# Performance work log

Measured on AMD Instinct MI355X. Metric: run time of the kernel, lower is better.

Reference implementation:

```python
import jax, jax.numpy as jnp
import numpy as np

B, N, EB, NA, DIM, NIT = 256, 128, 5, 64, 512, 3  # EB = n_bonds + 1 (channel 0 = no-bond, dropped)


def setup_inputs() -> dict:
    key = jax.random.key(0)
    ks = jax.random.split(key, 10)
    adj = jax.random.uniform(ks[0], (B, N, N, EB), dtype=jnp.float32)
    node = jax.random.normal(ks[1], (B, N, NA), dtype=jnp.float32)
    hidden = jnp.zeros((B, N, DIM), dtype=jnp.float32)  # accepted but unused by forward
    # nn.Linear default init: U(-1/sqrt(fan_in), 1/sqrt(fan_in))
    se = 1.0 / np.sqrt(NA)
    sd = 1.0 / np.sqrt(DIM)
    W_embed = jax.random.uniform(ks[2], (NA, DIM), minval=-se, maxval=se, dtype=jnp.float32)
    b_embed = jax.random.uniform(ks[3], (DIM,), minval=-se, maxval=se, dtype=jnp.float32)
    W_layers = jax.random.uniform(ks[4], (NIT, DIM, DIM), minval=-sd, maxval=sd, dtype=jnp.float32)
    b_layers = jax.random.uniform(ks[5], (NIT, DIM), minval=-sd, maxval=sd, dtype=jnp.float32)
    W_out = jax.random.uniform(ks[6], (DIM, 1), minval=-sd, maxval=sd, dtype=jnp.float32)
    b_out = jax.random.uniform(ks[7], (1,), minval=-sd, maxval=sd, dtype=jnp.float32)
    return {"adj": adj, "hidden": hidden, "node": node,
            "W_embed": W_embed, "b_embed": b_embed,
            "W_layers": W_layers, "b_layers": b_layers,
            "W_out": W_out, "b_out": b_out}


def reference(adj, hidden, node, W_embed, b_embed, W_layers, b_layers, W_out, b_out):
    # adj[:, :, :, 1:].permute(0, 3, 1, 2) -> [B, E, N, N]
    a = jnp.transpose(adj[..., 1:], (0, 3, 1, 2))
    h = node @ W_embed + b_embed  # [B, N, DIM]
    for i in range(NIT):  # WLSLinearLayer: relu(Linear(h + sum_e adj_e @ h))
        agg = jnp.einsum('benm,bmd->bnd', a, h)  # sum over bond types of neighbor aggregation
        h = jax.nn.relu((h + agg) @ W_layers[i] + b_layers[i])
    graph_repr = jnp.mean(h, axis=1)  # [B, DIM]
    logit = graph_repr @ W_out + b_out  # [B, 1], activation=None path
    return (logit, graph_repr)
```

## Files before the change

kernel.cpp:

```cpp
#include <hip/hip_runtime.h>
#include <hip/hip_bf16.h>


typedef __bf16 bf16;
typedef __bf16 bf16x4 __attribute__((ext_vector_type(4)));
typedef __bf16 bf16x8 __attribute__((ext_vector_type(8)));
typedef float floatx4 __attribute__((ext_vector_type(4)));

#define TBS 40
#define AS  136

__global__ __launch_bounds__(256) void k_pack(const float* __restrict__ We,
                                              const float* __restrict__ Wl,
                                              bf16* __restrict__ PWe,
                                              bf16* __restrict__ PWl) {
    __shared__ float S[512][17];
    int z = blockIdx.y, td = blockIdx.x;
    const float* src; bf16* dst; int K;
    if (z < 3) { src = Wl + (size_t)z * 262144; dst = PWl + (size_t)z * 262144; K = 512; }
    else       { src = We;                      dst = PWe;                      K = 64; }
    int tid = threadIdx.x;
    int x = tid & 15, y = tid >> 4;
    for (int kb = 0; kb < K; kb += 16) {
        int k = kb + y;
        S[k][x] = src[(size_t)k * 512 + td * 16 + x];
    }
    __syncthreads();
    int lane = tid & 63, w = tid >> 6, q = lane >> 4, l16 = lane & 15;
    int KT = K >> 5;
    for (int tk = w; tk < KT; tk += 4) {
        bf16x8 v;
#pragma unroll
        for (int j = 0; j < 8; j++) v[j] = (bf16)S[tk * 32 + q * 8 + j][l16];
        *(bf16x8*)&dst[(size_t)((td * KT + tk) * 64 + lane) * 8] = v;
    }
}

__global__ __launch_bounds__(1024, 4) void k_mega(
    const float* __restrict__ adj,
    const float* __restrict__ nodef,
    const bf16* __restrict__ PWe,
    const float* __restrict__ b_embed,
    const bf16* __restrict__ PWl,
    const float* __restrict__ b_layers,
    const float* __restrict__ W_out,
    const float* __restrict__ b_out,
    float* __restrict__ out)
{
    __shared__ __align__(16) char pool[141312];
    bf16* HT = (bf16*)pool;
    bf16* TB = (bf16*)(pool + 131072);

    const int b = blockIdx.x;
    const int tid = threadIdx.x;
    const int lane = tid & 63, wid = tid >> 6;
    const int q = lane >> 4, l16 = lane & 15;

    bf16* AhatL = (bf16*)pool;
    {
        const float4* srcb = (const float4*)(adj + (size_t)b * 81920);
#pragma unroll 2
        for (int p = 0; p < 4; p++) {
            int t = p * 1024 + tid;
            const float4* ptr = srcb + (size_t)t * 5;
            float4 v0 = ptr[0], v1 = ptr[1], v2 = ptr[2], v3 = ptr[3], v4 = ptr[4];
            float s0 = v0.y + v0.z + v0.w + v1.x;
            float s1 = v1.z + v1.w + v2.x + v2.y;
            float s2 = v2.w + v3.x + v3.y + v3.z;
            float s3 = v4.x + v4.y + v4.z + v4.w;
            int n = t >> 5, m0 = (t & 31) * 4;
            bf16x4 o;
            o[0] = (bf16)(s0 + ((n == m0 + 0) ? 1.f : 0.f));
            o[1] = (bf16)(s1 + ((n == m0 + 1) ? 1.f : 0.f));
            o[2] = (bf16)(s2 + ((n == m0 + 2) ? 1.f : 0.f));
            o[3] = (bf16)(s3 + ((n == m0 + 3) ? 1.f : 0.f));
            *(bf16x4*)&AhatL[n * AS + m0] = o;
        }
    }
    __syncthreads();

    const int dt = wid >> 3, ntw = wid & 7;
    bf16x8 ahf[4];
#pragma unroll
    for (int kk = 0; kk < 4; kk++)
        ahf[kk] = *(const bf16x8*)&AhatL[(ntw * 16 + l16) * AS + kk * 32 + q * 8];
    __syncthreads();

    {
        const int wmE = wid >> 3, wnE = wid & 7;
        const float* Ab = nodef + (size_t)b * 8192;
        floatx4 accE[4][4] = {};
#pragma unroll
        for (int kk = 0; kk < 2; kk++) {
            bf16x8 af[4], bfr[4];
#pragma unroll
            for (int mt = 0; mt < 4; mt++) {
                const float* srcp = Ab + (size_t)(wmE * 64 + mt * 16 + l16) * 64 + kk * 32 + q * 8;
                float4 x = *(const float4*)srcp;
                float4 y = *(const float4*)(srcp + 4);
                bf16x8 v;
                v[0] = (bf16)x.x; v[1] = (bf16)x.y; v[2] = (bf16)x.z; v[3] = (bf16)x.w;
                v[4] = (bf16)y.x; v[5] = (bf16)y.y; v[6] = (bf16)y.z; v[7] = (bf16)y.w;
                af[mt] = v;
            }
#pragma unroll
            for (int nt = 0; nt < 4; nt++) {
                int td = wnE * 4 + nt;
                bfr[nt] = *(const bf16x8*)&PWe[(size_t)((td * 2 + kk) * 64 + lane) * 8];
            }
#pragma unroll
            for (int mt = 0; mt < 4; mt++)
#pragma unroll
                for (int nt = 0; nt < 4; nt++)
                    accE[mt][nt] = __builtin_amdgcn_mfma_f32_16x16x32_bf16(af[mt], bfr[nt], accE[mt][nt], 0, 0, 0);
        }
#pragma unroll
        for (int mt = 0; mt < 4; mt++)
#pragma unroll
            for (int nt = 0; nt < 4; nt++) {
                int d = wnE * 64 + nt * 16 + l16;
                float bv = b_embed[d];
                int c = wmE * 8 + mt * 2 + (q >> 1);
                int off = ((c ^ (d & 15)) << 3) + (q & 1) * 4;
                bf16x4 pk;
#pragma unroll
                for (int r = 0; r < 4; r++) pk[r] = (bf16)(accE[mt][nt][r] + bv);
                *(bf16x4*)&HT[d * 128 + off] = pk;
            }
    }
    __syncthreads();

    const int nw = wid & 1, dw = wid >> 1;

    for (int it = 0; it < 3; it++) {
        const bf16* WT = PWl + (size_t)it * 262144;
        const float* bl = b_layers + it * 512;
        floatx4 acc[4][4] = {};

        for (int dc = 0; dc < 16; dc++) {
            bf16x8 bfr0 = *(const bf16x8*)&WT[(size_t)(((dw * 4 + 0) * 16 + dc) * 64 + lane) * 8];
            bf16x8 bfr1 = *(const bf16x8*)&WT[(size_t)(((dw * 4 + 1) * 16 + dc) * 64 + lane) * 8];

            floatx4 a1 = {};
            {
                int drow = dc * 32 + dt * 16 + l16;
#pragma unroll
                for (int kk = 0; kk < 4; kk++) {
                    int off = ((4 * kk + q) ^ (drow & 15)) << 3;
                    bf16x8 af = *(const bf16x8*)&HT[drow * 128 + off];
                    a1 = __builtin_amdgcn_mfma_f32_16x16x32_bf16(af, ahf[kk], a1, 0, 0, 0);
                }
            }
            {
                bf16x4 pk;
#pragma unroll
                for (int r = 0; r < 4; r++) pk[r] = (bf16)a1[r];
                *(bf16x4*)&TB[(ntw * 16 + l16) * TBS + dt * 16 + q * 4] = pk;
            }
            __syncthreads();

            bf16x8 af2[4];
#pragma unroll
            for (int mt = 0; mt < 4; mt++)
                af2[mt] = *(const bf16x8*)&TB[(nw * 64 + mt * 16 + l16) * TBS + q * 8];
            bf16x8 bfr2 = *(const bf16x8*)&WT[(size_t)(((dw * 4 + 2) * 16 + dc) * 64 + lane) * 8];
#pragma unroll
            for (int mt = 0; mt < 4; mt++)
                acc[mt][0] = __builtin_amdgcn_mfma_f32_16x16x32_bf16(af2[mt], bfr0, acc[mt][0], 0, 0, 0);
            bf16x8 bfr3 = *(const bf16x8*)&WT[(size_t)(((dw * 4 + 3) * 16 + dc) * 64 + lane) * 8];
#pragma unroll
            for (int mt = 0; mt < 4; mt++)
                acc[mt][1] = __builtin_amdgcn_mfma_f32_16x16x32_bf16(af2[mt], bfr1, acc[mt][1], 0, 0, 0);
#pragma unroll
            for (int mt = 0; mt < 4; mt++)
                acc[mt][2] = __builtin_amdgcn_mfma_f32_16x16x32_bf16(af2[mt], bfr2, acc[mt][2], 0, 0, 0);
#pragma unroll
            for (int mt = 0; mt < 4; mt++)
                acc[mt][3] = __builtin_amdgcn_mfma_f32_16x16x32_bf16(af2[mt], bfr3, acc[mt][3], 0, 0, 0);
            __syncthreads();
        }

        if (it < 2) {
#pragma unroll
            for (int nt = 0; nt < 4; nt++) {
                int dp = dw * 64 + nt * 16 + l16;
                float bv = bl[dp];
#pragma unroll
                for (int mt = 0; mt < 4; mt++) {
                    int c = nw * 8 + mt * 2 + (q >> 1);
                    int off = ((c ^ (dp & 15)) << 3) + (q & 1) * 4;
                    bf16x4 pk;
#pragma unroll
                    for (int r = 0; r < 4; r++) pk[r] = (bf16)fmaxf(acc[mt][nt][r] + bv, 0.f);
                    *(bf16x4*)&HT[dp * 128 + off] = pk;
                }
            }
            __syncthreads();
        } else {
            float* RsF = (float*)(pool + 131072);
#pragma unroll
            for (int nt = 0; nt < 4; nt++) {
                int dp = dw * 64 + nt * 16 + l16;
                float bv = bl[dp];
                float s = 0.f;
#pragma unroll
                for (int mt = 0; mt < 4; mt++)
#pragma unroll
                    for (int r = 0; r < 4; r++)
                        s += fmaxf(acc[mt][nt][r] + bv, 0.f);
                s += __shfl_down(s, 32);
                s += __shfl_down(s, 16);
                if (lane < 16) RsF[nw * 512 + dp] = s;
            }
        }
    }
    __syncthreads();

    float* RsF = (float*)(pool + 131072);
    float* lpF = (float*)(pool + 131072 + 4096);
    if (tid < 512) {
        float g = (RsF[tid] + RsF[512 + tid]) * (1.f / 128.f);
        out[256 + (size_t)b * 512 + tid] = g;
        lpF[tid] = g * W_out[tid];
    }
    __syncthreads();
    for (int s = 256; s > 0; s >>= 1) {
        if (tid < s) lpF[tid] += lpF[tid + s];
        __syncthreads();
    }
    if (tid == 0) out[b] = lpF[0] + b_out[0];
}

extern "C" void kernel_launch(void* const* d_in, const int* in_sizes, int n_in,
                              void* d_out, int out_size, void* d_ws, size_t ws_size,
                              hipStream_t stream) {
    const float* adj      = (const float*)d_in[0];
    const float* node     = (const float*)d_in[2];
    const float* W_embed  = (const float*)d_in[3];
    const float* b_embed  = (const float*)d_in[4];
    const float* W_layers = (const float*)d_in[5];
    const float* b_layers = (const float*)d_in[6];
    const float* W_out    = (const float*)d_in[7];
    const float* b_out    = (const float*)d_in[8];
    float* out = (float*)d_out;

    char* ws = (char*)d_ws;
    bf16* PWe = (bf16*)(ws);
    bf16* PWl = (bf16*)(ws + 65536);

    k_pack<<<dim3(32, 4), 256, 0, stream>>>(W_embed, W_layers, PWe, PWl);
    k_mega<<<256, 1024, 0, stream>>>(adj, node, PWe, b_embed, PWl, b_layers,
                                     W_out, b_out, out);
}
```

Measured before the change: 263.0 us.

## Compute full aggregation up front in place, removing per-chunk barriers in GEMM loop

Instead of computing each 32-wide d-chunk of the adjacency aggregation inside the W-layer GEMM loop and staging it through a small shared buffer with two barriers per chunk, each wave now computes its whole aggregation slice up front in registers. The result is written back over the hidden-state buffer in a transposed, swizzled n-major layout. The GEMM loop then reads A fragments straight from shared memory with no barriers inside it. This removes 32 block-wide syncs per layer and shrinks LDS, at the cost of 16 extra accumulator vectors per thread and less overlap between the aggregation and the GEMM.

```diff
diff --git a/kernel.cpp b/kernel.cpp
--- a/kernel.cpp
+++ b/kernel.cpp
@@ -7,7 +7,6 @@
 typedef __bf16 bf16x8 __attribute__((ext_vector_type(8)));
 typedef float floatx4 __attribute__((ext_vector_type(4)));
 
-#define TBS 40
 #define AS  136
 
 __global__ __launch_bounds__(256) void k_pack(const float* __restrict__ We,
@@ -47,9 +46,8 @@
     const float* __restrict__ b_out,
     float* __restrict__ out)
 {
-    __shared__ __align__(16) char pool[141312];
+    __shared__ __align__(16) char pool[137216];
     bf16* HT = (bf16*)pool;
-    bf16* TB = (bf16*)(pool + 131072);
 
     const int b = blockIdx.x;
     const int tid = threadIdx.x;
@@ -79,7 +77,7 @@
     }
     __syncthreads();
 
-    const int dt = wid >> 3, ntw = wid & 7;
+    const int ntw = wid & 7, dh = wid >> 3;
     bf16x8 ahf[4];
 #pragma unroll
     for (int kk = 0; kk < 4; kk++)
@@ -135,34 +133,44 @@
     for (int it = 0; it < 3; it++) {
         const bf16* WT = PWl + (size_t)it * 262144;
         const float* bl = b_layers + it * 512;
+
+        floatx4 at[16] = {};
+#pragma unroll
+        for (int dtile = 0; dtile < 16; dtile++) {
+            int drow = dh * 256 + dtile * 16 + l16;
+#pragma unroll
+            for (int kk = 0; kk < 4; kk++) {
+                int off = ((4 * kk + q) ^ (drow & 15)) << 3;
+                bf16x8 af = *(const bf16x8*)&HT[drow * 128 + off];
+                at[dtile] = __builtin_amdgcn_mfma_f32_16x16x32_bf16(af, ahf[kk], at[dtile], 0, 0, 0);
+            }
+        }
+        __syncthreads();
+        {
+            int n = ntw * 16 + l16;
+#pragma unroll
+            for (int dtile = 0; dtile < 16; dtile++) {
+                int c = dh * 32 + dtile * 2 + (q >> 1);
+                int off = ((c ^ l16) << 3) + (q & 1) * 4;
+                bf16x4 pk;
+#pragma unroll
+                for (int r = 0; r < 4; r++) pk[r] = (bf16)at[dtile][r];
+                *(bf16x4*)&HT[n * 512 + off] = pk;
+            }
+        }
+        __syncthreads();
+
         floatx4 acc[4][4] = {};
-
         for (int dc = 0; dc < 16; dc++) {
             bf16x8 bfr0 = *(const bf16x8*)&WT[(size_t)(((dw * 4 + 0) * 16 + dc) * 64 + lane) * 8];
             bf16x8 bfr1 = *(const bf16x8*)&WT[(size_t)(((dw * 4 + 1) * 16 + dc) * 64 + lane) * 8];
-
-            floatx4 a1 = {};
-            {
-                int drow = dc * 32 + dt * 16 + l16;
-#pragma unroll
-                for (int kk = 0; kk < 4; kk++) {
-                    int off = ((4 * kk + q) ^ (drow & 15)) << 3;
-                    bf16x8 af = *(const bf16x8*)&HT[drow * 128 + off];
-                    a1 = __builtin_amdgcn_mfma_f32_16x16x32_bf16(af, ahf[kk], a1, 0, 0, 0);
-                }
-            }
-            {
-                bf16x4 pk;
-#pragma unroll
-                for (int r = 0; r < 4; r++) pk[r] = (bf16)a1[r];
-                *(bf16x4*)&TB[(ntw * 16 + l16) * TBS + dt * 16 + q * 4] = pk;
-            }
-            __syncthreads();
-
             bf16x8 af2[4];
 #pragma unroll
-            for (int mt = 0; mt < 4; mt++)
-                af2[mt] = *(const bf16x8*)&TB[(nw * 64 + mt * 16 + l16) * TBS + q * 8];
+            for (int mt = 0; mt < 4; mt++) {
+                int nn = nw * 64 + mt * 16 + l16;
+                int c = (dc * 4 + q) ^ (nn & 15);
+                af2[mt] = *(const bf16x8*)&HT[nn * 512 + (c << 3)];
+            }
             bf16x8 bfr2 = *(const bf16x8*)&WT[(size_t)(((dw * 4 + 2) * 16 + dc) * 64 + lane) * 8];
 #pragma unroll
             for (int mt = 0; mt < 4; mt++)
@@ -177,10 +185,10 @@
 #pragma unroll
             for (int mt = 0; mt < 4; mt++)
                 acc[mt][3] = __builtin_amdgcn_mfma_f32_16x16x32_bf16(af2[mt], bfr3, acc[mt][3], 0, 0, 0);
+        }
+
+        if (it < 2) {
             __syncthreads();
-        }
-
-        if (it < 2) {
 #pragma unroll
             for (int nt = 0; nt < 4; nt++) {
                 int dp = dw * 64 + nt * 16 + l16;
```

New measurement: 282.0 us. 1.07x slower.
